# Kernel optimization log

Measured on AMD Instinct MI355X. Metric: run time of the kernel, lower is better.

## Reference

```python
import jax, jax.numpy as jnp
import numpy as np
from jax import lax

B, DIN, DOUT, DEPTH = 4096, 2048, 2048, 16


def setup_inputs() -> dict:
    key = jax.random.key(0)
    k1, k2, k3, k4 = jax.random.split(key, 4)
    return {
        "x": jax.random.normal(k1, (B, DIN), jnp.float32),
        "absolute_weights": jax.random.normal(k2, (DEPTH, DIN, DOUT), jnp.float32),
        "classical_weights": jax.random.normal(k3, (DIN, DOUT), jnp.float32),
        "classical_biases": jax.random.normal(k4, (DOUT,), jnp.float32),
    }


def _absolute_probs(W):
    # W: [depth, din, dout]; the torch code indexes W[d, j, g] with j over
    # output dims and g in {0,1,2} (3 gates per depth step).
    din = W.shape[1]
    dout = DOUT
    # angles per output j, flattened over (depth, gate): [dout, depth*3]
    ang = jnp.transpose(W[:, :dout, :3], (1, 0, 2)).reshape(dout, -1)
    s0 = jnp.ones((din,), W.dtype) / np.float32(np.sqrt(din))

    def step(s, a):
        # The dense "rotation" matrix built in torch is: diag=cos,
        # superdiag (wrapped) = -sin, subdiag (wrapped) = +sin, i.e.
        # (M s)[i] = cos*s[i] - sin*s[(i+1)%n] + sin*s[(i-1)%n].
        c, si = jnp.cos(a), jnp.sin(a)
        s_new = c * s - si * jnp.roll(s, -1) + si * jnp.roll(s, 1)
        return s_new, None

    def per_j(angs):
        s, _ = lax.scan(step, s0, angs)
        return jnp.abs(s[0]) ** 2

    return jax.vmap(per_j)(ang)  # [dout]


def reference(x, absolute_weights, classical_weights, classical_biases):
    classical = x @ classical_weights + classical_biases  # [B, dout]
    probs = _absolute_probs(absolute_weights)             # [dout], batch-independent
    return jnp.tanh(classical + probs[None, :])
```

## Files before the change

kernel.cpp:

```cpp
#include <hip/hip_runtime.h>
#include <math.h>

#define BATCH 4096
#define DIN   2048
#define DOUT  2048
#define DEPTH 16

typedef unsigned short u16;
typedef __attribute__((ext_vector_type(8))) short short8;
typedef __attribute__((ext_vector_type(4))) float f32x4;


__device__ static inline unsigned bf16_rn(float x) {
    unsigned u = __float_as_uint(x);
    return (u + 0x7FFFu + ((u >> 16) & 1u)) >> 16;
}

__device__ static inline float tanh_fast(float z) {
    float zc = fminf(fmaxf(z, -15.0f), 15.0f);
    float e = __builtin_amdgcn_exp2f(zc * 2.8853900817779268f);
    return (e - 1.0f) * __builtin_amdgcn_rcpf(e + 1.0f);
}

__device__ static inline void async16(u16* lds, const u16* g) {
    __builtin_amdgcn_global_load_lds(
        (const __attribute__((address_space(1))) void*)g,
        (__attribute__((address_space(3))) void*)lds, 16, 0, 0);
}

__global__ __launch_bounds__(256) void probs_kernel(const float* __restrict__ W,
                                                    float* __restrict__ probs) {
    int tid = threadIdx.x;
    int jl = tid >> 4, d = tid & 15;
    int j = blockIdx.x * 16 + jl;
    const float* p = W + (size_t)d * DIN * DOUT + (size_t)j * DOUT;
    float pr = cosf(p[0]) * cosf(p[1]) * cosf(p[2]);
#pragma unroll
    for (int off = 1; off < 16; off <<= 1) pr *= __shfl_xor(pr, off, 16);
    if (d == 0) probs[j] = pr * pr * (1.0f / (float)DIN);
}

__global__ __launch_bounds__(256) void convert_x_kernel(const float* __restrict__ x,
                                                        u16* __restrict__ xh,
                                                        u16* __restrict__ xl) {
    int i = (blockIdx.x * 256 + threadIdx.x) * 4;
    float4 v = *(const float4*)(x + i);
    ushort4 h, l;
    float vv[4] = {v.x, v.y, v.z, v.w};
    u16 hh[4], ll[4];
#pragma unroll
    for (int c = 0; c < 4; ++c) {
        unsigned hb = bf16_rn(vv[c]);
        hh[c] = (u16)hb;
        float r = vv[c] - __uint_as_float(hb << 16);
        ll[c] = (u16)bf16_rn(r);
    }
    h.x = hh[0]; h.y = hh[1]; h.z = hh[2]; h.w = hh[3];
    l.x = ll[0]; l.y = ll[1]; l.z = ll[2]; l.w = ll[3];
    *(ushort4*)(xh + i) = h;
    *(ushort4*)(xl + i) = l;
}

__global__ __launch_bounds__(256) void transpose_w_kernel(const float* __restrict__ W,
                                                          u16* __restrict__ wh,
                                                          u16* __restrict__ wl) {
    __shared__ float t[32][33];
    int n0 = blockIdx.x * 32, k0 = blockIdx.y * 32;
    int tx = threadIdx.x & 31, ty = threadIdx.x >> 5;
#pragma unroll
    for (int i = 0; i < 4; ++i)
        t[ty + i * 8][tx] = W[(size_t)(k0 + ty + i * 8) * DOUT + n0 + tx];
    __syncthreads();
#pragma unroll
    for (int i = 0; i < 4; ++i) {
        float v = t[tx][ty + i * 8];
        size_t o = (size_t)(n0 + ty + i * 8) * DIN + k0 + tx;
        unsigned hb = bf16_rn(v);
        wh[o] = (u16)hb;
        float r = v - __uint_as_float(hb << 16);
        wl[o] = (u16)bf16_rn(r);
    }
}

__global__ __launch_bounds__(256, 2) void gemm_mfma_kernel(
    const u16* __restrict__ xh, const u16* __restrict__ xl,
    const u16* __restrict__ wh, const u16* __restrict__ wl,
    const float* __restrict__ bias, const float* __restrict__ probs,
    float* __restrict__ C)
{
    __shared__ u16 lds[2][16384];

    const int tid = threadIdx.x;
    const int lane = tid & 63;
    const int wave = tid >> 6;

    const int bid = blockIdx.x;
    const int swz = (bid & 7) * 64 + (bid >> 3);
    const int bR = (swz & 31) * 128;
    const int bC = (swz >> 5) * 128;

    const u16* gsrc = (wave == 0) ? xh + (size_t)bR * DIN
                    : (wave == 1) ? xl + (size_t)bR * DIN
                    : (wave == 2) ? wh + (size_t)bC * DIN
                                  : wl + (size_t)bC * DIN;

    int goff[8];
#pragma unroll
    for (int i = 0; i < 8; ++i) {
        int row = i * 16 + (lane >> 2);
        int lq = (lane & 3) ^ ((row >> 1) & 3);
        goff[i] = row * DIN + lq * 8;
    }

    const int wm = wave >> 1, wn = wave & 1;
    const int colL = lane & 15, quad = lane >> 4;

    int aoff[4], boff[4];
#pragma unroll
    for (int mt = 0; mt < 4; ++mt) {
        int r = wm * 64 + mt * 16 + colL;
        aoff[mt] = r * 32 + (quad ^ ((r >> 1) & 3)) * 8;
    }
#pragma unroll
    for (int nt = 0; nt < 4; ++nt) {
        int r = wn * 64 + nt * 16 + colL;
        boff[nt] = 8192 + r * 32 + (quad ^ ((r >> 1) & 3)) * 8;
    }

    u16* st0 = &lds[0][0] + wave * 4096;
    u16* st1 = st0 + 16384;

    f32x4 acc[4][4];
#pragma unroll
    for (int mt = 0; mt < 4; ++mt)
#pragma unroll
        for (int nt = 0; nt < 4; ++nt) acc[mt][nt] = (f32x4){0.f, 0.f, 0.f, 0.f};

#pragma unroll
    for (int i = 0; i < 8; ++i) async16(st0 + i * 512, gsrc + goff[i]);
    __syncthreads();

#pragma unroll 2
    for (int t = 0; t < 63; ++t) {
        const int cur = t & 1;
        const u16* Lb = &lds[0][0] + cur * 16384;

        short8 ah[4], al[4], bh[4], bl[4];
#pragma unroll
        for (int mt = 0; mt < 4; ++mt) {
            ah[mt] = *(const short8*)(Lb + aoff[mt]);
            al[mt] = *(const short8*)(Lb + 4096 + aoff[mt]);
        }
#pragma unroll
        for (int nt = 0; nt < 4; ++nt) {
            bh[nt] = *(const short8*)(Lb + boff[nt]);
            bl[nt] = *(const short8*)(Lb + 4096 + boff[nt]);
        }

        {
            u16* st = cur ? st0 : st1;
            const int k1 = (t + 1) * 32;
#pragma unroll
            for (int i = 0; i < 8; ++i) async16(st + i * 512, gsrc + goff[i] + k1);
        }

#pragma unroll
        for (int mt = 0; mt < 4; ++mt)
#pragma unroll
            for (int nt = 0; nt < 4; ++nt) {
                acc[mt][nt] = __builtin_amdgcn_mfma_f32_16x16x32_bf16(
                    ah[mt], bh[nt], acc[mt][nt], 0, 0, 0);
                acc[mt][nt] = __builtin_amdgcn_mfma_f32_16x16x32_bf16(
                    ah[mt], bl[nt], acc[mt][nt], 0, 0, 0);
                acc[mt][nt] = __builtin_amdgcn_mfma_f32_16x16x32_bf16(
                    al[mt], bh[nt], acc[mt][nt], 0, 0, 0);
            }

        __syncthreads();
    }

    {
        const u16* Lb = &lds[0][0] + 16384;
        short8 ah[4], al[4], bh[4], bl[4];
#pragma unroll
        for (int mt = 0; mt < 4; ++mt) {
            ah[mt] = *(const short8*)(Lb + aoff[mt]);
            al[mt] = *(const short8*)(Lb + 4096 + aoff[mt]);
        }
#pragma unroll
        for (int nt = 0; nt < 4; ++nt) {
            bh[nt] = *(const short8*)(Lb + boff[nt]);
            bl[nt] = *(const short8*)(Lb + 4096 + boff[nt]);
        }
#pragma unroll
        for (int mt = 0; mt < 4; ++mt)
#pragma unroll
            for (int nt = 0; nt < 4; ++nt) {
                acc[mt][nt] = __builtin_amdgcn_mfma_f32_16x16x32_bf16(
                    ah[mt], bh[nt], acc[mt][nt], 0, 0, 0);
                acc[mt][nt] = __builtin_amdgcn_mfma_f32_16x16x32_bf16(
                    ah[mt], bl[nt], acc[mt][nt], 0, 0, 0);
                acc[mt][nt] = __builtin_amdgcn_mfma_f32_16x16x32_bf16(
                    al[mt], bh[nt], acc[mt][nt], 0, 0, 0);
            }
    }

    float bp[4];
#pragma unroll
    for (int nt = 0; nt < 4; ++nt) {
        int c = bC + wn * 64 + nt * 16 + colL;
        bp[nt] = bias[c] + probs[c];
    }
#pragma unroll
    for (int mt = 0; mt < 4; ++mt)
#pragma unroll
        for (int nt = 0; nt < 4; ++nt) {
            int c = bC + wn * 64 + nt * 16 + colL;
#pragma unroll
            for (int reg = 0; reg < 4; ++reg) {
                int r = bR + wm * 64 + mt * 16 + quad * 4 + reg;
                C[(size_t)r * DOUT + c] = tanh_fast(acc[mt][nt][reg] + bp[nt]);
            }
        }
}

__global__ __launch_bounds__(256) void gemm_tanh_kernel(
    const float* __restrict__ A, const float* __restrict__ Bw,
    const float* __restrict__ bias, const float* __restrict__ probs,
    float* __restrict__ C)
{
    __shared__ float As[16][128 + 4];
    __shared__ float Bs[16][128 + 4];
    const int tid = threadIdx.x;
    const int block_row = blockIdx.y * 128;
    const int block_col = blockIdx.x * 128;
    const int tr = (tid >> 4) << 3;
    const int tc = (tid & 15) << 3;
    const int a_row = tid >> 2;
    const int a_col = (tid & 3) << 2;
    const int b_row = tid >> 5;
    const int b_col = (tid & 31) << 2;
    const float* Aptr0 = A + (size_t)(block_row + a_row) * DIN + a_col;
    const float* Aptr1 = Aptr0 + (size_t)64 * DIN;
    const float* Bptr0 = Bw + (size_t)b_row * DOUT + block_col + b_col;
    const float* Bptr1 = Bptr0 + (size_t)8 * DOUT;
    float acc[8][8] = {};
    for (int k0 = 0; k0 < DIN; k0 += 16) {
        float4 a0 = *(const float4*)(Aptr0 + k0);
        float4 a1 = *(const float4*)(Aptr1 + k0);
        float4 b0 = *(const float4*)(Bptr0 + (size_t)k0 * DOUT);
        float4 b1 = *(const float4*)(Bptr1 + (size_t)k0 * DOUT);
        __syncthreads();
        As[a_col + 0][a_row] = a0.x;
        As[a_col + 1][a_row] = a0.y;
        As[a_col + 2][a_row] = a0.z;
        As[a_col + 3][a_row] = a0.w;
        As[a_col + 0][a_row + 64] = a1.x;
        As[a_col + 1][a_row + 64] = a1.y;
        As[a_col + 2][a_row + 64] = a1.z;
        As[a_col + 3][a_row + 64] = a1.w;
        *(float4*)&Bs[b_row][b_col]     = b0;
        *(float4*)&Bs[b_row + 8][b_col] = b1;
        __syncthreads();
#pragma unroll
        for (int kk = 0; kk < 16; ++kk) {
            float ar[8], br[8];
#pragma unroll
            for (int i = 0; i < 8; ++i) ar[i] = As[kk][tr + i];
#pragma unroll
            for (int i = 0; i < 8; ++i) br[i] = Bs[kk][tc + i];
#pragma unroll
            for (int i = 0; i < 8; ++i)
#pragma unroll
                for (int jj = 0; jj < 8; ++jj)
                    acc[i][jj] = fmaf(ar[i], br[jj], acc[i][jj]);
        }
    }
    float bp[8];
#pragma unroll
    for (int jj = 0; jj < 8; ++jj)
        bp[jj] = bias[block_col + tc + jj] + probs[block_col + tc + jj];
#pragma unroll
    for (int i = 0; i < 8; ++i) {
        float* crow = C + (size_t)(block_row + tr + i) * DOUT + block_col + tc;
#pragma unroll
        for (int jj = 0; jj < 8; ++jj)
            crow[jj] = tanh_fast(acc[i][jj] + bp[jj]);
    }
}

extern "C" void kernel_launch(void* const* d_in, const int* in_sizes, int n_in,
                              void* d_out, int out_size, void* d_ws, size_t ws_size,
                              hipStream_t stream) {
    const float* x  = (const float*)d_in[0];
    const float* W  = (const float*)d_in[1];
    const float* cw = (const float*)d_in[2];
    const float* cb = (const float*)d_in[3];
    float* out = (float*)d_out;

    const size_t PROBS_B = 8192;
    const size_t XSZ = (size_t)BATCH * DIN;
    const size_t WSZ = (size_t)DIN * DOUT;
    const size_t need = PROBS_B + 2 * XSZ * 2 + 2 * WSZ * 2;

    float* probs = (float*)d_ws;
    probs_kernel<<<DOUT / 16, 256, 0, stream>>>(W, probs);

    if (ws_size >= need) {
        u16* xh = (u16*)((char*)d_ws + PROBS_B);
        u16* xl = xh + XSZ;
        u16* wh = xl + XSZ;
        u16* wl = wh + WSZ;

        convert_x_kernel<<<XSZ / 4 / 256, 256, 0, stream>>>(x, xh, xl);
        transpose_w_kernel<<<dim3(DOUT / 32, DIN / 32), 256, 0, stream>>>(cw, wh, wl);

        gemm_mfma_kernel<<<512, 256, 0, stream>>>(xh, xl, wh, wl, cb, probs, out);
    } else {
        dim3 grid(DOUT / 128, BATCH / 128);
        gemm_tanh_kernel<<<grid, 256, 0, stream>>>(x, cw, cb, probs, out);
    }
}
```

Before: 435.0 us.

## Use 8-wave blocks with triple-buffered LDS and a single barrier per step

The GEMM block grows from 4 to 8 waves, so each wave computes a 64x32 sub-tile and issues half as many async loads. LDS becomes a three-stage ring with prefetch two steps ahead, guarded by an explicit vmcnt wait and one barrier per iteration instead of the end-of-loop __syncthreads. s_setprio raises wave priority around the MFMA block. The goal is to hide global-load latency and raise MFMA utilization, at the cost of 96KB LDS per block, which may limit how many blocks fit per CU, and of fragile hand-written wait counts.

Result: no change. 439.7 us (+1.1%).

```diff
diff --git a/kernel.cpp b/kernel.cpp
--- a/kernel.cpp
+++ b/kernel.cpp
@@ -82,13 +82,13 @@
     }
 }
 
-__global__ __launch_bounds__(256, 2) void gemm_mfma_kernel(
+__global__ __launch_bounds__(512, 2) void gemm_mfma_kernel(
     const u16* __restrict__ xh, const u16* __restrict__ xl,
     const u16* __restrict__ wh, const u16* __restrict__ wl,
     const float* __restrict__ bias, const float* __restrict__ probs,
     float* __restrict__ C)
 {
-    __shared__ u16 lds[2][16384];
+    __shared__ __align__(16) u16 lds[3][16384];
 
     const int tid = threadIdx.x;
     const int lane = tid & 63;
@@ -99,75 +99,83 @@
     const int bR = (swz & 31) * 128;
     const int bC = (swz >> 5) * 128;
 
-    const u16* gsrc = (wave == 0) ? xh + (size_t)bR * DIN
-                    : (wave == 1) ? xl + (size_t)bR * DIN
-                    : (wave == 2) ? wh + (size_t)bC * DIN
-                                  : wl + (size_t)bC * DIN;
-
-    int goff[8];
-#pragma unroll
-    for (int i = 0; i < 8; ++i) {
+    const int arr = wave >> 1, half = wave & 1;
+    const u16* gsrc = (arr == 0) ? xh + (size_t)bR * DIN
+                    : (arr == 1) ? xl + (size_t)bR * DIN
+                    : (arr == 2) ? wh + (size_t)bC * DIN
+                                 : wl + (size_t)bC * DIN;
+    gsrc += (size_t)(half * 64) * DIN;
+
+    int goff[4];
+#pragma unroll
+    for (int i = 0; i < 4; ++i) {
         int row = i * 16 + (lane >> 2);
-        int lq = (lane & 3) ^ ((row >> 1) & 3);
+        int fullrow = half * 64 + row;
+        int lq = (lane & 3) ^ ((fullrow >> 1) & 3);
         goff[i] = row * DIN + lq * 8;
     }
-
-    const int wm = wave >> 1, wn = wave & 1;
+    const int stoff = arr * 4096 + half * 2048;
+
+    const int wm = wave >> 2, wn = wave & 3;
     const int colL = lane & 15, quad = lane >> 4;
 
-    int aoff[4], boff[4];
+    int aoff[4], boff[2];
 #pragma unroll
     for (int mt = 0; mt < 4; ++mt) {
         int r = wm * 64 + mt * 16 + colL;
         aoff[mt] = r * 32 + (quad ^ ((r >> 1) & 3)) * 8;
     }
 #pragma unroll
-    for (int nt = 0; nt < 4; ++nt) {
-        int r = wn * 64 + nt * 16 + colL;
+    for (int nt = 0; nt < 2; ++nt) {
+        int r = wn * 32 + nt * 16 + colL;
         boff[nt] = 8192 + r * 32 + (quad ^ ((r >> 1) & 3)) * 8;
     }
 
-    u16* st0 = &lds[0][0] + wave * 4096;
-    u16* st1 = st0 + 16384;
-
-    f32x4 acc[4][4];
+    f32x4 acc[4][2];
 #pragma unroll
     for (int mt = 0; mt < 4; ++mt)
 #pragma unroll
-        for (int nt = 0; nt < 4; ++nt) acc[mt][nt] = (f32x4){0.f, 0.f, 0.f, 0.f};
-
-#pragma unroll
-    for (int i = 0; i < 8; ++i) async16(st0 + i * 512, gsrc + goff[i]);
-    __syncthreads();
-
-#pragma unroll 2
+        for (int nt = 0; nt < 2; ++nt) acc[mt][nt] = (f32x4){0.f, 0.f, 0.f, 0.f};
+
+#pragma unroll
+    for (int i = 0; i < 4; ++i) async16(&lds[0][0] + stoff + i * 512, gsrc + goff[i]);
+#pragma unroll
+    for (int i = 0; i < 4; ++i) async16(&lds[1][0] + stoff + i * 512, gsrc + goff[i] + 32);
+
+#pragma unroll 1
     for (int t = 0; t < 63; ++t) {
-        const int cur = t & 1;
-        const u16* Lb = &lds[0][0] + cur * 16384;
-
-        short8 ah[4], al[4], bh[4], bl[4];
+        const int cur = t % 3;
+
+        asm volatile("s_waitcnt vmcnt(4)" ::: "memory");
+        __builtin_amdgcn_s_barrier();
+        asm volatile("" ::: "memory");
+        __builtin_amdgcn_sched_barrier(0);
+
+        if (t < 62) {
+            u16* st = &lds[(t + 2) % 3][0] + stoff;
+            const int kk = (t + 2) * 32;
+#pragma unroll
+            for (int i = 0; i < 4; ++i) async16(st + i * 512, gsrc + goff[i] + kk);
+        }
+
+        const u16* Lb = &lds[cur][0];
+        short8 ah[4], al[4], bh[2], bl[2];
 #pragma unroll
         for (int mt = 0; mt < 4; ++mt) {
             ah[mt] = *(const short8*)(Lb + aoff[mt]);
             al[mt] = *(const short8*)(Lb + 4096 + aoff[mt]);
         }
 #pragma unroll
-        for (int nt = 0; nt < 4; ++nt) {
+        for (int nt = 0; nt < 2; ++nt) {
             bh[nt] = *(const short8*)(Lb + boff[nt]);
             bl[nt] = *(const short8*)(Lb + 4096 + boff[nt]);
         }
 
-        {
-            u16* st = cur ? st0 : st1;
-            const int k1 = (t + 1) * 32;
-#pragma unroll
-            for (int i = 0; i < 8; ++i) async16(st + i * 512, gsrc + goff[i] + k1);
-        }
-
+        __builtin_amdgcn_s_setprio(1);
 #pragma unroll
         for (int mt = 0; mt < 4; ++mt)
 #pragma unroll
-            for (int nt = 0; nt < 4; ++nt) {
+            for (int nt = 0; nt < 2; ++nt) {
                 acc[mt][nt] = __builtin_amdgcn_mfma_f32_16x16x32_bf16(
                     ah[mt], bh[nt], acc[mt][nt], 0, 0, 0);
                 acc[mt][nt] = __builtin_amdgcn_mfma_f32_16x16x32_bf16(
@@ -175,27 +183,31 @@
                 acc[mt][nt] = __builtin_amdgcn_mfma_f32_16x16x32_bf16(
                     al[mt], bh[nt], acc[mt][nt], 0, 0, 0);
             }
-
-        __syncthreads();
+        __builtin_amdgcn_s_setprio(0);
     }
 
     {
-        const u16* Lb = &lds[0][0] + 16384;
-        short8 ah[4], al[4], bh[4], bl[4];
+        asm volatile("s_waitcnt vmcnt(0)" ::: "memory");
+        __builtin_amdgcn_s_barrier();
+        asm volatile("" ::: "memory");
+        __builtin_amdgcn_sched_barrier(0);
+
+        const u16* Lb = &lds[0][0];
+        short8 ah[4], al[4], bh[2], bl[2];
 #pragma unroll
         for (int mt = 0; mt < 4; ++mt) {
             ah[mt] = *(const short8*)(Lb + aoff[mt]);
             al[mt] = *(const short8*)(Lb + 4096 + aoff[mt]);
         }
 #pragma unroll
-        for (int nt = 0; nt < 4; ++nt) {
+        for (int nt = 0; nt < 2; ++nt) {
             bh[nt] = *(const short8*)(Lb + boff[nt]);
             bl[nt] = *(const short8*)(Lb + 4096 + boff[nt]);
         }
 #pragma unroll
         for (int mt = 0; mt < 4; ++mt)
 #pragma unroll
-            for (int nt = 0; nt < 4; ++nt) {
+            for (int nt = 0; nt < 2; ++nt) {
                 acc[mt][nt] = __builtin_amdgcn_mfma_f32_16x16x32_bf16(
                     ah[mt], bh[nt], acc[mt][nt], 0, 0, 0);
                 acc[mt][nt] = __builtin_amdgcn_mfma_f32_16x16x32_bf16(
@@ -205,17 +217,17 @@
             }
     }
 
-    float bp[4];
-#pragma unroll
-    for (int nt = 0; nt < 4; ++nt) {
-        int c = bC + wn * 64 + nt * 16 + colL;
+    float bp[2];
+#pragma unroll
+    for (int nt = 0; nt < 2; ++nt) {
+        int c = bC + wn * 32 + nt * 16 + colL;
         bp[nt] = bias[c] + probs[c];
     }
 #pragma unroll
     for (int mt = 0; mt < 4; ++mt)
 #pragma unroll
-        for (int nt = 0; nt < 4; ++nt) {
-            int c = bC + wn * 64 + nt * 16 + colL;
+        for (int nt = 0; nt < 2; ++nt) {
+            int c = bC + wn * 32 + nt * 16 + colL;
 #pragma unroll
             for (int reg = 0; reg < 4; ++reg) {
                 int r = bR + wm * 64 + mt * 16 + quad * 4 + reg;
@@ -315,7 +327,7 @@
         convert_x_kernel<<<XSZ / 4 / 256, 256, 0, stream>>>(x, xh, xl);
         transpose_w_kernel<<<dim3(DOUT / 32, DIN / 32), 256, 0, stream>>>(cw, wh, wl);
 
-        gemm_mfma_kernel<<<512, 256, 0, stream>>>(xh, xl, wh, wl, cb, probs, out);
+        gemm_mfma_kernel<<<512, 512, 0, stream>>>(xh, xl, wh, wl, cb, probs, out);
     } else {
         dim3 grid(DOUT / 128, BATCH / 128);
         gemm_tanh_kernel<<<grid, 256, 0, stream>>>(x, cw, cb, probs, out);
```

## Fuse prepass kernels, enlarge GEMM tile to 256x128, add triple-buffered pipeline

Applied to the files above, without the earlier changes.

Merges the probs, x-split and weight transpose/split kernels into one launch to cut launch overhead. The MFMA GEMM tile grows from 128x128 to 256x128 with 256 blocks at one block per CU, so each B fragment is reused across more rows. LDS moves to a three-stage ring with async loads issued two steps ahead, explicit vmcnt waits plus a single barrier per step, and s_setprio around the MFMA block. The cost is higher register pressure from 32 accumulator tiles, lower occupancy, and a 256-block grid that may not fill every CU evenly.

Result: no change. 430.2 us (-1.1%).

```diff
diff --git a/kernel.cpp b/kernel.cpp
--- a/kernel.cpp
+++ b/kernel.cpp
@@ -26,6 +26,62 @@
     __builtin_amdgcn_global_load_lds(
         (const __attribute__((address_space(1))) void*)g,
         (__attribute__((address_space(3))) void*)lds, 16, 0, 0);
+}
+
+__global__ __launch_bounds__(256) void prepass_kernel(
+    const float* __restrict__ x, const float* __restrict__ W,
+    const float* __restrict__ cw,
+    float* __restrict__ probs,
+    u16* __restrict__ xh, u16* __restrict__ xl,
+    u16* __restrict__ wh, u16* __restrict__ wl)
+{
+    const int b = blockIdx.x;
+    const int tid = threadIdx.x;
+
+    if (b < 128) {
+        int jl = tid >> 4, d = tid & 15;
+        int j = b * 16 + jl;
+        const float* p = W + (size_t)d * DIN * DOUT + (size_t)j * DOUT;
+        float pr = cosf(p[0]) * cosf(p[1]) * cosf(p[2]);
+#pragma unroll
+        for (int off = 1; off < 16; off <<= 1) pr *= __shfl_xor(pr, off, 16);
+        if (d == 0) probs[j] = pr * pr * (1.0f / (float)DIN);
+    } else if (b < 8320) {
+        int i = ((b - 128) * 256 + tid) * 4;
+        float4 v = *(const float4*)(x + i);
+        float vv[4] = {v.x, v.y, v.z, v.w};
+        u16 hh[4], ll[4];
+#pragma unroll
+        for (int c = 0; c < 4; ++c) {
+            unsigned hb = bf16_rn(vv[c]);
+            hh[c] = (u16)hb;
+            float r = vv[c] - __uint_as_float(hb << 16);
+            ll[c] = (u16)bf16_rn(r);
+        }
+        ushort4 h, l;
+        h.x = hh[0]; h.y = hh[1]; h.z = hh[2]; h.w = hh[3];
+        l.x = ll[0]; l.y = ll[1]; l.z = ll[2]; l.w = ll[3];
+        *(ushort4*)(xh + i) = h;
+        *(ushort4*)(xl + i) = l;
+    } else {
+        __shared__ float t[32][33];
+        int b2 = b - 8320;
+        int n0 = (b2 & 63) * 32, k0 = (b2 >> 6) * 32;
+        int tx = tid & 31, ty = tid >> 5;
+#pragma unroll
+        for (int i = 0; i < 4; ++i)
+            t[ty + i * 8][tx] = cw[(size_t)(k0 + ty + i * 8) * DOUT + n0 + tx];
+        __syncthreads();
+#pragma unroll
+        for (int i = 0; i < 4; ++i) {
+            float v = t[tx][ty + i * 8];
+            size_t o = (size_t)(n0 + ty + i * 8) * DIN + k0 + tx;
+            unsigned hb = bf16_rn(v);
+            wh[o] = (u16)hb;
+            float r = v - __uint_as_float(hb << 16);
+            wl[o] = (u16)bf16_rn(r);
+        }
+    }
 }
 
 __global__ __launch_bounds__(256) void probs_kernel(const float* __restrict__ W,
@@ -40,116 +96,86 @@
     if (d == 0) probs[j] = pr * pr * (1.0f / (float)DIN);
 }
 
-__global__ __launch_bounds__(256) void convert_x_kernel(const float* __restrict__ x,
-                                                        u16* __restrict__ xh,
-                                                        u16* __restrict__ xl) {
-    int i = (blockIdx.x * 256 + threadIdx.x) * 4;
-    float4 v = *(const float4*)(x + i);
-    ushort4 h, l;
-    float vv[4] = {v.x, v.y, v.z, v.w};
-    u16 hh[4], ll[4];
-#pragma unroll
-    for (int c = 0; c < 4; ++c) {
-        unsigned hb = bf16_rn(vv[c]);
-        hh[c] = (u16)hb;
-        float r = vv[c] - __uint_as_float(hb << 16);
-        ll[c] = (u16)bf16_rn(r);
-    }
-    h.x = hh[0]; h.y = hh[1]; h.z = hh[2]; h.w = hh[3];
-    l.x = ll[0]; l.y = ll[1]; l.z = ll[2]; l.w = ll[3];
-    *(ushort4*)(xh + i) = h;
-    *(ushort4*)(xl + i) = l;
-}
-
-__global__ __launch_bounds__(256) void transpose_w_kernel(const float* __restrict__ W,
-                                                          u16* __restrict__ wh,
-                                                          u16* __restrict__ wl) {
-    __shared__ float t[32][33];
-    int n0 = blockIdx.x * 32, k0 = blockIdx.y * 32;
-    int tx = threadIdx.x & 31, ty = threadIdx.x >> 5;
-#pragma unroll
-    for (int i = 0; i < 4; ++i)
-        t[ty + i * 8][tx] = W[(size_t)(k0 + ty + i * 8) * DOUT + n0 + tx];
-    __syncthreads();
-#pragma unroll
-    for (int i = 0; i < 4; ++i) {
-        float v = t[tx][ty + i * 8];
-        size_t o = (size_t)(n0 + ty + i * 8) * DIN + k0 + tx;
-        unsigned hb = bf16_rn(v);
-        wh[o] = (u16)hb;
-        float r = v - __uint_as_float(hb << 16);
-        wl[o] = (u16)bf16_rn(r);
-    }
-}
-
-__global__ __launch_bounds__(256, 2) void gemm_mfma_kernel(
+__global__ __launch_bounds__(256, 1) void gemm_mfma_kernel(
     const u16* __restrict__ xh, const u16* __restrict__ xl,
     const u16* __restrict__ wh, const u16* __restrict__ wl,
     const float* __restrict__ bias, const float* __restrict__ probs,
     float* __restrict__ C)
 {
-    __shared__ u16 lds[2][16384];
+    __shared__ __align__(16) u16 lds[3][24576];
 
     const int tid = threadIdx.x;
     const int lane = tid & 63;
     const int wave = tid >> 6;
 
     const int bid = blockIdx.x;
-    const int swz = (bid & 7) * 64 + (bid >> 3);
-    const int bR = (swz & 31) * 128;
-    const int bC = (swz >> 5) * 128;
-
-    const u16* gsrc = (wave == 0) ? xh + (size_t)bR * DIN
-                    : (wave == 1) ? xl + (size_t)bR * DIN
-                    : (wave == 2) ? wh + (size_t)bC * DIN
-                                  : wl + (size_t)bC * DIN;
-
-    int goff[8];
-#pragma unroll
-    for (int i = 0; i < 8; ++i) {
-        int row = i * 16 + (lane >> 2);
-        int lq = (lane & 3) ^ ((row >> 1) & 3);
-        goff[i] = row * DIN + lq * 8;
-    }
+    const int swz = (bid & 7) * 32 + (bid >> 3);
+    const int bR = (swz & 15) * 256;
+    const int bC = (swz >> 4) * 128;
+
+    const u16* psrc[12];
+#pragma unroll
+    for (int j = 0; j < 12; ++j) {
+        int c = wave * 12 + j;
+        const u16* base;
+        int lrow;
+        if (c < 16)      { base = xh + (size_t)bR * DIN; lrow = c * 16 + (lane >> 2); }
+        else if (c < 32) { base = xl + (size_t)bR * DIN; lrow = (c - 16) * 16 + (lane >> 2); }
+        else if (c < 40) { base = wh + (size_t)bC * DIN; lrow = (c - 32) * 16 + (lane >> 2); }
+        else             { base = wl + (size_t)bC * DIN; lrow = (c - 40) * 16 + (lane >> 2); }
+        int lq = (lane & 3) ^ ((lrow >> 1) & 3);
+        psrc[j] = base + (size_t)lrow * DIN + lq * 8;
+    }
+    const int dst0 = wave * 12 * 512;
 
     const int wm = wave >> 1, wn = wave & 1;
     const int colL = lane & 15, quad = lane >> 4;
 
-    int aoff[4], boff[4];
-#pragma unroll
-    for (int mt = 0; mt < 4; ++mt) {
-        int r = wm * 64 + mt * 16 + colL;
+    int aoff[8], boff[4];
+#pragma unroll
+    for (int mt = 0; mt < 8; ++mt) {
+        int r = wm * 128 + mt * 16 + colL;
         aoff[mt] = r * 32 + (quad ^ ((r >> 1) & 3)) * 8;
     }
 #pragma unroll
     for (int nt = 0; nt < 4; ++nt) {
         int r = wn * 64 + nt * 16 + colL;
-        boff[nt] = 8192 + r * 32 + (quad ^ ((r >> 1) & 3)) * 8;
-    }
-
-    u16* st0 = &lds[0][0] + wave * 4096;
-    u16* st1 = st0 + 16384;
-
-    f32x4 acc[4][4];
-#pragma unroll
-    for (int mt = 0; mt < 4; ++mt)
+        boff[nt] = 16384 + r * 32 + (quad ^ ((r >> 1) & 3)) * 8;
+    }
+
+    f32x4 acc[8][4];
+#pragma unroll
+    for (int mt = 0; mt < 8; ++mt)
 #pragma unroll
         for (int nt = 0; nt < 4; ++nt) acc[mt][nt] = (f32x4){0.f, 0.f, 0.f, 0.f};
 
 #pragma unroll
-    for (int i = 0; i < 8; ++i) async16(st0 + i * 512, gsrc + goff[i]);
-    __syncthreads();
-
-#pragma unroll 2
+    for (int j = 0; j < 12; ++j) async16(&lds[0][0] + dst0 + j * 512, psrc[j]);
+#pragma unroll
+    for (int j = 0; j < 12; ++j) async16(&lds[1][0] + dst0 + j * 512, psrc[j] + 32);
+
+#pragma unroll 1
     for (int t = 0; t < 63; ++t) {
-        const int cur = t & 1;
-        const u16* Lb = &lds[0][0] + cur * 16384;
-
-        short8 ah[4], al[4], bh[4], bl[4];
-#pragma unroll
-        for (int mt = 0; mt < 4; ++mt) {
+        const int cur = t % 3;
+
+        asm volatile("s_waitcnt vmcnt(12)" ::: "memory");
+        __builtin_amdgcn_s_barrier();
+        asm volatile("" ::: "memory");
+        __builtin_amdgcn_sched_barrier(0);
+
+        if (t < 62) {
+            u16* st = &lds[(t + 2) % 3][0] + dst0;
+            const int kk = (t + 2) * 32;
+#pragma unroll
+            for (int j = 0; j < 12; ++j) async16(st + j * 512, psrc[j] + kk);
+        }
+
+        const u16* Lb = &lds[cur][0];
+        short8 ah[8], al[8], bh[4], bl[4];
+#pragma unroll
+        for (int mt = 0; mt < 8; ++mt) {
             ah[mt] = *(const short8*)(Lb + aoff[mt]);
-            al[mt] = *(const short8*)(Lb + 4096 + aoff[mt]);
+            al[mt] = *(const short8*)(Lb + 8192 + aoff[mt]);
         }
 #pragma unroll
         for (int nt = 0; nt < 4; ++nt) {
@@ -157,15 +183,9 @@
             bl[nt] = *(const short8*)(Lb + 4096 + boff[nt]);
         }
 
-        {
-            u16* st = cur ? st0 : st1;
-            const int k1 = (t + 1) * 32;
-#pragma unroll
-            for (int i = 0; i < 8; ++i) async16(st + i * 512, gsrc + goff[i] + k1);
-        }
-
-#pragma unroll
-        for (int mt = 0; mt < 4; ++mt)
+        __builtin_amdgcn_s_setprio(1);
+#pragma unroll
+        for (int mt = 0; mt < 8; ++mt)
 #pragma unroll
             for (int nt = 0; nt < 4; ++nt) {
                 acc[mt][nt] = __builtin_amdgcn_mfma_f32_16x16x32_bf16(
@@ -175,17 +195,21 @@
                 acc[mt][nt] = __builtin_amdgcn_mfma_f32_16x16x32_bf16(
                     al[mt], bh[nt], acc[mt][nt], 0, 0, 0);
             }
-
-        __syncthreads();
+        __builtin_amdgcn_s_setprio(0);
     }
 
     {
-        const u16* Lb = &lds[0][0] + 16384;
-        short8 ah[4], al[4], bh[4], bl[4];
-#pragma unroll
-        for (int mt = 0; mt < 4; ++mt) {
+        asm volatile("s_waitcnt vmcnt(0)" ::: "memory");
+        __builtin_amdgcn_s_barrier();
+        asm volatile("" ::: "memory");
+        __builtin_amdgcn_sched_barrier(0);
+
+        const u16* Lb = &lds[0][0];
+        short8 ah[8], al[8], bh[4], bl[4];
+#pragma unroll
+        for (int mt = 0; mt < 8; ++mt) {
             ah[mt] = *(const short8*)(Lb + aoff[mt]);
-            al[mt] = *(const short8*)(Lb + 4096 + aoff[mt]);
+            al[mt] = *(const short8*)(Lb + 8192 + aoff[mt]);
         }
 #pragma unroll
         for (int nt = 0; nt < 4; ++nt) {
@@ -193,7 +217,7 @@
             bl[nt] = *(const short8*)(Lb + 4096 + boff[nt]);
         }
 #pragma unroll
-        for (int mt = 0; mt < 4; ++mt)
+        for (int mt = 0; mt < 8; ++mt)
 #pragma unroll
             for (int nt = 0; nt < 4; ++nt) {
                 acc[mt][nt] = __builtin_amdgcn_mfma_f32_16x16x32_bf16(
@@ -212,13 +236,13 @@
         bp[nt] = bias[c] + probs[c];
     }
 #pragma unroll
-    for (int mt = 0; mt < 4; ++mt)
+    for (int mt = 0; mt < 8; ++mt)
 #pragma unroll
         for (int nt = 0; nt < 4; ++nt) {
             int c = bC + wn * 64 + nt * 16 + colL;
 #pragma unroll
             for (int reg = 0; reg < 4; ++reg) {
-                int r = bR + wm * 64 + mt * 16 + quad * 4 + reg;
+                int r = bR + wm * 128 + mt * 16 + quad * 4 + reg;
                 C[(size_t)r * DOUT + c] = tanh_fast(acc[mt][nt][reg] + bp[nt]);
             }
         }
@@ -304,7 +328,6 @@
     const size_t need = PROBS_B + 2 * XSZ * 2 + 2 * WSZ * 2;
 
     float* probs = (float*)d_ws;
-    probs_kernel<<<DOUT / 16, 256, 0, stream>>>(W, probs);
 
     if (ws_size >= need) {
         u16* xh = (u16*)((char*)d_ws + PROBS_B);
@@ -312,11 +335,11 @@
         u16* wh = xl + XSZ;
         u16* wl = wh + WSZ;
 
-        convert_x_kernel<<<XSZ / 4 / 256, 256, 0, stream>>>(x, xh, xl);
-        transpose_w_kernel<<<dim3(DOUT / 32, DIN / 32), 256, 0, stream>>>(cw, wh, wl);
-
-        gemm_mfma_kernel<<<512, 256, 0, stream>>>(xh, xl, wh, wl, cb, probs, out);
+        prepass_kernel<<<12416, 256, 0, stream>>>(x, W, cw, probs, xh, xl, wh, wl);
+
+        gemm_mfma_kernel<<<256, 256, 0, stream>>>(xh, xl, wh, wl, cb, probs, out);
     } else {
+        probs_kernel<<<DOUT / 16, 256, 0, stream>>>(W, probs);
         dim3 grid(DOUT / 128, BATCH / 128);
         gemm_tanh_kernel<<<grid, 256, 0, stream>>>(x, cw, cb, probs, out);
     }
```
